# Optimization experiments

Hardware: AMD Instinct MI355X
Metric: run time of the kernel (lower is better)

## Reference

```python
import jax, jax.numpy as jnp
import numpy as np

K = 16  # number of nearest neighbors (includes self)


def setup_inputs() -> dict:
    key = jax.random.key(0)
    ks = jax.random.split(key, 12)
    B, N, D = 8, 4096, 3
    H, G, A = 128, 16, 32
    s = lambda k, shape, fan: jax.random.normal(k, shape, jnp.float32) / np.sqrt(fan)
    return {
        "pos": jax.random.normal(ks[0], (B, N, D), jnp.float32),
        "goal": jax.random.normal(ks[1], (B, G), jnp.float32),
        # local_encoder: Linear(2D,64) -> ReLU -> Linear(64,H) -> ReLU
        "W1": s(ks[2], (2 * D, 64), 2 * D), "b1": jnp.zeros((64,), jnp.float32),
        "W2": s(ks[3], (64, H), 64), "b2": jnp.zeros((H,), jnp.float32),
        # FiLM conditioning from goal
        "Wg": s(ks[4], (G, H), G), "bg": jnp.zeros((H,), jnp.float32),
        "Wb": s(ks[5], (G, H), G), "bb": jnp.zeros((H,), jnp.float32),
        # to_affordance: Linear(H, A) -> ReLU
        "Wa": s(ks[6], (H, A), H), "ba": jnp.zeros((A,), jnp.float32),
    }


def reference(pos, goal, W1, b1, W2, b2, Wg, bg, Wb, bb, Wa, ba):
    # pos: (B, N, D)
    # Squared pairwise distances via the Gram trick (monotone in true distance,
    # so k-NN indices match torch.cdist + topk(largest=False)).
    sq = jnp.sum(pos * pos, axis=-1)                      # (B, N)
    d2 = sq[:, :, None] + sq[:, None, :] - 2.0 * jnp.einsum("bnd,bmd->bnm", pos, pos)
    d2 = jnp.maximum(d2, 0.0)                             # (B, N, N)
    _, idx = jax.lax.top_k(-d2, K)                        # smallest K -> (B, N, K)

    # Gather neighbor coordinates: neighbors[b, i, j] = pos[b, idx[b, i, j]]
    neighbors = jax.vmap(lambda p, i: p[i])(pos, idx)     # (B, N, K, D)
    # mean of relative offsets == mean(neighbors) - pos
    local_context = neighbors.mean(axis=2) - pos          # (B, N, D)

    x = jnp.concatenate([pos, local_context], axis=-1)    # (B, N, 2D)
    h = jax.nn.relu(x @ W1 + b1)
    features = jax.nn.relu(h @ W2 + b2)                   # (B, N, H)

    gamma = (goal @ Wg + bg)[:, None, :]                  # (B, 1, H)
    beta = (goal @ Wb + bb)[:, None, :]
    features = gamma * features + beta

    return jax.nn.relu(features @ Wa + ba)                # (B, N, A)
```

## Files before the change

### kernel.cpp

```cpp
#include <hip/hip_runtime.h>
#include <math.h>

#define NPTS 4096
#define QTR  1024
#define KNN  16
#define H_DIM 128
#define HID1 64
#define A_DIM 32
#define G_DIM 16

#define BUF_ROWS 16
#define FLUSH_AT 8
#define GROUP 8
#define EPS 3e-4f

typedef unsigned long long u64;


#define SWAP_ST(k)                                                         \
    { bool sw_ = best[k] < best[k-1];                                      \
      u64 lo_ = sw_ ? best[k] : best[k-1];                                 \
      u64 hi_ = sw_ ? best[k-1] : best[k];                                 \
      best[k-1] = lo_; best[k] = hi_; }

#define INSERT_KEY(keyv)                                                   \
    { best[15] = (keyv);                                                   \
      SWAP_ST(15) SWAP_ST(14) SWAP_ST(13) SWAP_ST(12) SWAP_ST(11)          \
      SWAP_ST(10) SWAP_ST(9)  SWAP_ST(8)  SWAP_ST(7)  SWAP_ST(6)           \
      SWAP_ST(5)  SWAP_ST(4)  SWAP_ST(3)  SWAP_ST(2)  SWAP_ST(1) }

#define CE(i, j)                                                           \
    { u64 x_ = m[i], y_ = m[j];                                            \
      bool sw_ = y_ < x_;                                                  \
      m[i] = sw_ ? y_ : x_; m[j] = sw_ ? x_ : y_; }

__global__ __launch_bounds__(256, 2) void knn_film_mlp_kernel(
    const float* __restrict__ pos, const float* __restrict__ goal,
    const float* __restrict__ W1, const float* __restrict__ b1,
    const float* __restrict__ W2, const float* __restrict__ b2,
    const float* __restrict__ Wg, const float* __restrict__ bg,
    const float* __restrict__ Wb, const float* __restrict__ bb,
    const float* __restrict__ Wa, const float* __restrict__ ba,
    float* __restrict__ out)
{
    __shared__ float4 sp[NPTS];
    __shared__ unsigned short bufi[BUF_ROWS][256];
    __shared__ unsigned short pubi[2][KNN][64];
    __shared__ float gam[H_DIM], bet[H_DIM];
    __shared__ float4 lc[64];

    const int tid  = threadIdx.x;
    const int lane = tid & 63;
    const int wid  = tid >> 6;
    const int b     = blockIdx.x >> 6;
    const int chunk = blockIdx.x & 63;
    const int q     = chunk * 64 + lane;

    const float* pb = pos + (size_t)b * NPTS * 3;
    for (int j = tid; j < NPTS; j += 256) {
        float x = pb[j * 3 + 0];
        float y = pb[j * 3 + 1];
        float z = pb[j * 3 + 2];
        float sq = __fadd_rn(__fadd_rn(__fmul_rn(x, x), __fmul_rn(y, y)),
                             __fmul_rn(z, z));
        sp[j] = make_float4(x, y, z, sq);
    }
    if (tid < H_DIM) {
        const float* gl = goal + b * G_DIM;
        float sg = bg[tid];
        float sb = bb[tid];
        #pragma unroll
        for (int g = 0; g < G_DIM; ++g) {
            float gv = gl[g];
            sg = fmaf(gv, Wg[g * H_DIM + tid], sg);
            sb = fmaf(gv, Wb[g * H_DIM + tid], sb);
        }
        gam[tid] = sg;
        bet[tid] = sb;
    }
    __syncthreads();

    const float4 me = sp[q];
    const float nx = -2.0f * me.x, ny = -2.0f * me.y, nz = -2.0f * me.z;

#define CAND_D2(c)                                                             \
    __fsub_rn(__fadd_rn(me.w, (c).w),                                          \
              __fmul_rn(2.0f,                                                  \
                        __fadd_rn(__fadd_rn(__fmul_rn(me.x, (c).x),            \
                                            __fmul_rn(me.y, (c).y)),           \
                                  __fmul_rn(me.z, (c).z))))

    u64 best[KNN];
    #pragma unroll
    for (int k = 0; k < KNN; ++k) best[k] = 0xFFFFFFFFFFFFFFFFull;

    const int jbase = wid * QTR;

    for (int j = jbase; j < jbase + KNN; ++j) {
        float4 c = sp[j];
        float d2 = fmaxf(CAND_D2(c), 0.0f);
        u64 key = ((u64)__float_as_uint(d2) << 32) | (unsigned)j;
        INSERT_KEY(key);
    }
    float thrm = (__uint_as_float((unsigned)(best[15] >> 32)) - me.w) + EPS;
    int cnt = 0;

#define FLUSH()                                                                \
    { int t = 0;                                                               \
      while (__any(t < cnt)) {                                                 \
          int j = bufi[t][tid] & (NPTS - 1);                                   \
          float4 c = sp[j];                                                    \
          float d2 = fmaxf(CAND_D2(c), 0.0f);                                  \
          u64 key = ((u64)__float_as_uint(d2) << 32) | (unsigned)j;            \
          if ((t < cnt) && (key < best[15])) { INSERT_KEY(key); }              \
          t++;                                                                 \
      }                                                                        \
      cnt = 0;                                                                 \
      thrm = (__uint_as_float((unsigned)(best[15] >> 32)) - me.w) + EPS; }

    for (int j0 = jbase + KNN; j0 < jbase + QTR; j0 += GROUP) {
        #pragma unroll
        for (int jj = 0; jj < GROUP; ++jj) {
            const int j = j0 + jj;
            float4 c = sp[j];
            float s = fmaf(nx, c.x, fmaf(ny, c.y, fmaf(nz, c.z, c.w)));
            bool pass = s < thrm;
            bufi[cnt][tid] = (unsigned short)j;
            cnt += pass ? 1 : 0;
        }
        if (__any(cnt >= FLUSH_AT)) FLUSH();
    }
    FLUSH();

    float* pubd = (float*)&bufi[0][0];

#define PUBLISH(l)                                                             \
    _Pragma("unroll")                                                          \
    for (int k = 0; k < KNN; ++k) {                                            \
        pubd[(l) * 1024 + k * 64 + lane] =                                     \
            __uint_as_float((unsigned)(best[k] >> 32));                        \
        pubi[l][k][lane] = (unsigned short)(best[k] & 0xFFFFu);                \
    }

#define MERGE_FROM(l)                                                          \
    { u64 m[16];                                                               \
      _Pragma("unroll")                                                        \
      for (int i = 0; i < 16; ++i) {                                           \
          int kk = 15 - i;                                                     \
          u64 bk = ((u64)__float_as_uint(pubd[(l) * 1024 + kk * 64 + lane])    \
                    << 32) | (u64)pubi[l][kk][lane];                           \
          m[i] = best[i] < bk ? best[i] : bk;                                  \
      }                                                                        \
      CE(0,8) CE(1,9) CE(2,10) CE(3,11) CE(4,12) CE(5,13) CE(6,14) CE(7,15)    \
      CE(0,4) CE(1,5) CE(2,6) CE(3,7) CE(8,12) CE(9,13) CE(10,14) CE(11,15)    \
      CE(0,2) CE(1,3) CE(4,6) CE(5,7) CE(8,10) CE(9,11) CE(12,14) CE(13,15)    \
      CE(0,1) CE(2,3) CE(4,5) CE(6,7) CE(8,9) CE(10,11) CE(12,13) CE(14,15)    \
      _Pragma("unroll")                                                        \
      for (int i = 0; i < 16; ++i) best[i] = m[i]; }

    __syncthreads();
    if (wid >= 2) PUBLISH(wid - 2);
    __syncthreads();
    if (wid == 0) MERGE_FROM(0);
    if (wid == 1) { MERGE_FROM(1); PUBLISH(1); }
    __syncthreads();
    if (wid == 0) {
        MERGE_FROM(1);
        float sx = 0.0f, sy = 0.0f, sz = 0.0f;
        #pragma unroll
        for (int k = 0; k < KNN; ++k) {
            float4 nb = sp[(unsigned)(best[k] & 0xFFFFu)];
            sx += nb.x; sy += nb.y; sz += nb.z;
        }
        const float inv = 1.0f / (float)KNN;
        lc[lane] = make_float4(sx * inv - me.x, sy * inv - me.y,
                               sz * inv - me.z, 0.0f);
    }
    __syncthreads();

    {
        float4 l4 = lc[lane];
        const float x3 = l4.x, x4 = l4.y, x5 = l4.z;
        float h[HID1];
        #pragma unroll
        for (int c = 0; c < HID1; ++c) {
            float a = b1[c];
            a = fmaf(me.x, W1[0 * HID1 + c], a);
            a = fmaf(me.y, W1[1 * HID1 + c], a);
            a = fmaf(me.z, W1[2 * HID1 + c], a);
            a = fmaf(x3,   W1[3 * HID1 + c], a);
            a = fmaf(x4,   W1[4 * HID1 + c], a);
            a = fmaf(x5,   W1[5 * HID1 + c], a);
            h[c] = fmaxf(a, 0.0f);
        }
        float acc[A_DIM];
        #pragma unroll
        for (int a = 0; a < A_DIM; ++a) acc[a] = 0.0f;
        const int ci = wid;
        #pragma unroll 4
        for (int cc = 0; cc < 32; ++cc) {
            const int c = ci * 32 + cc;
            float s = b2[c];
            #pragma unroll
            for (int k = 0; k < HID1; ++k) s = fmaf(h[k], W2[k * H_DIM + c], s);
            float f = fmaf(gam[c], fmaxf(s, 0.0f), bet[c]);
            const float* wac = Wa + c * A_DIM;
            #pragma unroll
            for (int a = 0; a < A_DIM; ++a) acc[a] = fmaf(f, wac[a], acc[a]);
        }
        float* P = (float*)sp;
        #pragma unroll
        for (int a = 0; a < A_DIM; ++a) P[(ci * A_DIM + a) * 64 + lane] = acc[a];
    }
    __syncthreads();

    {
        const float* P = (const float*)sp;
        const int qi = tid >> 2, a0 = (tid & 3) * 8;
        float o[8];
        #pragma unroll
        for (int a = 0; a < 8; ++a) {
            float ssum = ba[a0 + a];
            #pragma unroll
            for (int c4 = 0; c4 < 4; ++c4)
                ssum += P[(c4 * A_DIM + a0 + a) * 64 + qi];
            o[a] = fmaxf(ssum, 0.0f);
        }
        float4* op4 = (float4*)(out + ((size_t)b * NPTS + chunk * 64 + qi) * A_DIM + a0);
        op4[0] = make_float4(o[0], o[1], o[2], o[3]);
        op4[1] = make_float4(o[4], o[5], o[6], o[7]);
    }
#undef CAND_D2
#undef FLUSH
#undef PUBLISH
#undef MERGE_FROM
}

extern "C" void kernel_launch(void* const* d_in, const int* in_sizes, int n_in,
                              void* d_out, int out_size, void* d_ws, size_t ws_size,
                              hipStream_t stream) {
    const float* pos  = (const float*)d_in[0];
    const float* goal = (const float*)d_in[1];
    const float* W1   = (const float*)d_in[2];
    const float* b1   = (const float*)d_in[3];
    const float* W2   = (const float*)d_in[4];
    const float* b2   = (const float*)d_in[5];
    const float* Wg   = (const float*)d_in[6];
    const float* bg   = (const float*)d_in[7];
    const float* Wb   = (const float*)d_in[8];
    const float* bb   = (const float*)d_in[9];
    const float* Wa   = (const float*)d_in[10];
    const float* ba   = (const float*)d_in[11];
    float* out = (float*)d_out;

    const int B = in_sizes[0] / (NPTS * 3);
    dim3 grid(B * 64);
    dim3 block(256);
    hipLaunchKernelGGL(knn_film_mlp_kernel, grid, block, 0, stream,
                       pos, goal, W1, b1, W2, b2, Wg, bg, Wb, bb, Wa, ba, out);
}
```

Baseline: 262.7 us.

## Split candidate scan across eight waves with shared atomic kNN threshold

Doubles the block to 512 threads so each of eight waves scans an eighth of the candidate points for the same 64 queries. The per-query pruning threshold now lives in shared memory and is tightened with atomicMin, so every wave prunes with the best bound found by any wave. Partial top-16 lists are merged through a double-buffered publish/merge chain, and the MLP and reduction stages are re-split across eight waves. Buffer and group sizes shrink to fit LDS. In exchange there is a longer serial merge chain, more barriers, and register pressure under launch_bounds(512,4).

```diff
diff --git a/kernel.cpp b/kernel.cpp
--- a/kernel.cpp
+++ b/kernel.cpp
@@ -2,19 +2,20 @@
 #include <math.h>
 
 #define NPTS 4096
-#define QTR  1024
+#define EIG  512
 #define KNN  16
 #define H_DIM 128
 #define HID1 64
 #define A_DIM 32
 #define G_DIM 16
 
-#define BUF_ROWS 16
-#define FLUSH_AT 8
-#define GROUP 8
+#define BUF_ROWS 7
+#define FLUSH_AT 4
+#define GROUP 4
 #define EPS 3e-4f
 
 typedef unsigned long long u64;
+typedef unsigned short u16;
 
 
 #define SWAP_ST(k)                                                         \
@@ -34,7 +35,7 @@
       bool sw_ = y_ < x_;                                                  \
       m[i] = sw_ ? y_ : x_; m[j] = sw_ ? x_ : y_; }
 
-__global__ __launch_bounds__(256, 2) void knn_film_mlp_kernel(
+__global__ __launch_bounds__(512, 4) void knn_film_mlp_kernel(
     const float* __restrict__ pos, const float* __restrict__ goal,
     const float* __restrict__ W1, const float* __restrict__ b1,
     const float* __restrict__ W2, const float* __restrict__ b2,
@@ -44,10 +45,9 @@
     float* __restrict__ out)
 {
     __shared__ float4 sp[NPTS];
-    __shared__ unsigned short bufi[BUF_ROWS][256];
-    __shared__ unsigned short pubi[2][KNN][64];
-    __shared__ float gam[H_DIM], bet[H_DIM];
-    __shared__ float4 lc[64];
+    __shared__ int    pool[12544 / 4];
+    __shared__ float  gam[H_DIM], bet[H_DIM];
+    __shared__ float  lcx[64], lcy[64], lcz[64];
 
     const int tid  = threadIdx.x;
     const int lane = tid & 63;
@@ -56,8 +56,13 @@
     const int chunk = blockIdx.x & 63;
     const int q     = chunk * 64 + lane;
 
+    u16* sbuf = (u16*)pool;
+    int* sthr = pool + (12288 / 4);
+
+    if (tid < 64) sthr[tid] = 0x7F800000;
+
     const float* pb = pos + (size_t)b * NPTS * 3;
-    for (int j = tid; j < NPTS; j += 256) {
+    for (int j = tid; j < NPTS; j += 512) {
         float x = pb[j * 3 + 0];
         float y = pb[j * 3 + 1];
         float z = pb[j * 3 + 2];
@@ -94,7 +99,7 @@
     #pragma unroll
     for (int k = 0; k < KNN; ++k) best[k] = 0xFFFFFFFFFFFFFFFFull;
 
-    const int jbase = wid * QTR;
+    const int jbase = wid * EIG;
 
     for (int j = jbase; j < jbase + KNN; ++j) {
         float4 c = sp[j];
@@ -102,13 +107,14 @@
         u64 key = ((u64)__float_as_uint(d2) << 32) | (unsigned)j;
         INSERT_KEY(key);
     }
-    float thrm = (__uint_as_float((unsigned)(best[15] >> 32)) - me.w) + EPS;
+    atomicMin(&sthr[lane], (int)(unsigned)(best[15] >> 32));
+
     int cnt = 0;
 
 #define FLUSH()                                                                \
     { int t = 0;                                                               \
       while (__any(t < cnt)) {                                                 \
-          int j = bufi[t][tid] & (NPTS - 1);                                   \
+          int j = sbuf[t * 512 + tid] & (NPTS - 1);                            \
           float4 c = sp[j];                                                    \
           float d2 = fmaxf(CAND_D2(c), 0.0f);                                  \
           u64 key = ((u64)__float_as_uint(d2) << 32) | (unsigned)j;            \
@@ -116,39 +122,42 @@
           t++;                                                                 \
       }                                                                        \
       cnt = 0;                                                                 \
-      thrm = (__uint_as_float((unsigned)(best[15] >> 32)) - me.w) + EPS; }
-
-    for (int j0 = jbase + KNN; j0 < jbase + QTR; j0 += GROUP) {
+      unsigned b15_ = (unsigned)(best[15] >> 32);                              \
+      if (b15_ < 0x7F800000u) atomicMin(&sthr[lane], (int)b15_); }
+
+    for (int j0 = jbase + KNN; j0 < jbase + EIG; j0 += GROUP) {
+        float sv = __int_as_float(sthr[lane]);
+        float tm = (sv - me.w) + EPS;
         #pragma unroll
         for (int jj = 0; jj < GROUP; ++jj) {
             const int j = j0 + jj;
             float4 c = sp[j];
             float s = fmaf(nx, c.x, fmaf(ny, c.y, fmaf(nz, c.z, c.w)));
-            bool pass = s < thrm;
-            bufi[cnt][tid] = (unsigned short)j;
+            bool pass = s < tm;
+            sbuf[cnt * 512 + tid] = (u16)j;
             cnt += pass ? 1 : 0;
         }
         if (__any(cnt >= FLUSH_AT)) FLUSH();
     }
     FLUSH();
 
-    float* pubd = (float*)&bufi[0][0];
-
-#define PUBLISH(l)                                                             \
+#define PUBLISH(s)                                                             \
     _Pragma("unroll")                                                          \
     for (int k = 0; k < KNN; ++k) {                                            \
-        pubd[(l) * 1024 + k * 64 + lane] =                                     \
+        ((float*)pool)[(s) * 1536 + k * 64 + lane] =                           \
             __uint_as_float((unsigned)(best[k] >> 32));                        \
-        pubi[l][k][lane] = (unsigned short)(best[k] & 0xFFFFu);                \
-    }
-
-#define MERGE_FROM(l)                                                          \
+        ((u16*)pool)[(s) * 3072 + 2048 + k * 64 + lane] =                      \
+            (u16)(best[k] & 0xFFFFu);                                          \
+    }
+
+#define MERGE_FROM(s)                                                          \
     { u64 m[16];                                                               \
       _Pragma("unroll")                                                        \
       for (int i = 0; i < 16; ++i) {                                           \
           int kk = 15 - i;                                                     \
-          u64 bk = ((u64)__float_as_uint(pubd[(l) * 1024 + kk * 64 + lane])    \
-                    << 32) | (u64)pubi[l][kk][lane];                           \
+          u64 bk = ((u64)__float_as_uint(                                      \
+                        ((float*)pool)[(s) * 1536 + kk * 64 + lane]) << 32)    \
+                 | (u64)((u16*)pool)[(s) * 3072 + 2048 + kk * 64 + lane];      \
           m[i] = best[i] < bk ? best[i] : bk;                                  \
       }                                                                        \
       CE(0,8) CE(1,9) CE(2,10) CE(3,11) CE(4,12) CE(5,13) CE(6,14) CE(7,15)    \
@@ -159,13 +168,28 @@
       for (int i = 0; i < 16; ++i) best[i] = m[i]; }
 
     __syncthreads();
-    if (wid >= 2) PUBLISH(wid - 2);
+    if (wid == 1) PUBLISH(0);
+    if (wid == 2) PUBLISH(1);
     __syncthreads();
     if (wid == 0) MERGE_FROM(0);
-    if (wid == 1) { MERGE_FROM(1); PUBLISH(1); }
+    __syncthreads();
+    if (wid == 0) MERGE_FROM(1);
+    if (wid == 3) PUBLISH(0);
+    __syncthreads();
+    if (wid == 0) MERGE_FROM(0);
+    if (wid == 4) PUBLISH(1);
+    __syncthreads();
+    if (wid == 0) MERGE_FROM(1);
+    if (wid == 5) PUBLISH(0);
+    __syncthreads();
+    if (wid == 0) MERGE_FROM(0);
+    if (wid == 6) PUBLISH(1);
+    __syncthreads();
+    if (wid == 0) MERGE_FROM(1);
+    if (wid == 7) PUBLISH(0);
     __syncthreads();
     if (wid == 0) {
-        MERGE_FROM(1);
+        MERGE_FROM(0);
         float sx = 0.0f, sy = 0.0f, sz = 0.0f;
         #pragma unroll
         for (int k = 0; k < KNN; ++k) {
@@ -173,14 +197,14 @@
             sx += nb.x; sy += nb.y; sz += nb.z;
         }
         const float inv = 1.0f / (float)KNN;
-        lc[lane] = make_float4(sx * inv - me.x, sy * inv - me.y,
-                               sz * inv - me.z, 0.0f);
+        lcx[lane] = sx * inv - me.x;
+        lcy[lane] = sy * inv - me.y;
+        lcz[lane] = sz * inv - me.z;
     }
     __syncthreads();
 
     {
-        float4 l4 = lc[lane];
-        const float x3 = l4.x, x4 = l4.y, x5 = l4.z;
+        const float x3 = lcx[lane], x4 = lcy[lane], x5 = lcz[lane];
         float h[HID1];
         #pragma unroll
         for (int c = 0; c < HID1; ++c) {
@@ -196,10 +220,10 @@
         float acc[A_DIM];
         #pragma unroll
         for (int a = 0; a < A_DIM; ++a) acc[a] = 0.0f;
-        const int ci = wid;
+        const int c0 = wid * 16;
         #pragma unroll 4
-        for (int cc = 0; cc < 32; ++cc) {
-            const int c = ci * 32 + cc;
+        for (int cc = 0; cc < 16; ++cc) {
+            const int c = c0 + cc;
             float s = b2[c];
             #pragma unroll
             for (int k = 0; k < HID1; ++k) s = fmaf(h[k], W2[k * H_DIM + c], s);
@@ -210,25 +234,25 @@
         }
         float* P = (float*)sp;
         #pragma unroll
-        for (int a = 0; a < A_DIM; ++a) P[(ci * A_DIM + a) * 64 + lane] = acc[a];
+        for (int a = 0; a < A_DIM; ++a) P[(wid * A_DIM + a) * 64 + lane] = acc[a];
     }
     __syncthreads();
 
     {
         const float* P = (const float*)sp;
-        const int qi = tid >> 2, a0 = (tid & 3) * 8;
-        float o[8];
-        #pragma unroll
-        for (int a = 0; a < 8; ++a) {
-            float ssum = ba[a0 + a];
+        const int qi = tid & 63;
+        const int a0 = (tid >> 6) * 4;
+        float o[4];
+        #pragma unroll
+        for (int i = 0; i < 4; ++i) {
+            float ssum = ba[a0 + i];
             #pragma unroll
-            for (int c4 = 0; c4 < 4; ++c4)
-                ssum += P[(c4 * A_DIM + a0 + a) * 64 + qi];
-            o[a] = fmaxf(ssum, 0.0f);
+            for (int w = 0; w < 8; ++w)
+                ssum += P[(w * A_DIM + a0 + i) * 64 + qi];
+            o[i] = fmaxf(ssum, 0.0f);
         }
         float4* op4 = (float4*)(out + ((size_t)b * NPTS + chunk * 64 + qi) * A_DIM + a0);
-        op4[0] = make_float4(o[0], o[1], o[2], o[3]);
-        op4[1] = make_float4(o[4], o[5], o[6], o[7]);
+        *op4 = make_float4(o[0], o[1], o[2], o[3]);
     }
 #undef CAND_D2
 #undef FLUSH
@@ -255,7 +279,7 @@
 
     const int B = in_sizes[0] / (NPTS * 3);
     dim3 grid(B * 64);
-    dim3 block(256);
+    dim3 block(512);
     hipLaunchKernelGGL(knn_film_mlp_kernel, grid, block, 0, stream,
                        pos, goal, W1, b1, W2, b2, Wg, bg, Wb, bb, Wa, ba, out);
 }
```

Result: slower. 282.7 us (+7.6%).

## Share pruning threshold across waves via LDS atomicMin and use bitmask windows

Applied to the files above, without the earlier changes.

Swaps the per-thread candidate buffer and flush loop for 16-candidate windows that collect passing candidates into a bitmask and insert them right away. The four waves scanning different quarters of the point set for the same query now share a running k-th-distance threshold through an LDS atomicMin, so each wave prunes against the tightest bound found so far. The aim is fewer insertion-sort calls and less shared-memory buffer traffic. In exchange it adds an atomic and an LDS threshold read per window, and wave divergence inside the mask loop.

```diff
diff --git a/kernel.cpp b/kernel.cpp
--- a/kernel.cpp
+++ b/kernel.cpp
@@ -9,12 +9,13 @@
 #define A_DIM 32
 #define G_DIM 16
 
-#define BUF_ROWS 16
-#define FLUSH_AT 8
-#define GROUP 8
+#define WARMUP 16
+#define WSZ 16
+#define NWIN ((QTR - WARMUP) / WSZ)
 #define EPS 3e-4f
 
 typedef unsigned long long u64;
+typedef unsigned short u16;
 
 
 #define SWAP_ST(k)                                                         \
@@ -44,10 +45,11 @@
     float* __restrict__ out)
 {
     __shared__ float4 sp[NPTS];
-    __shared__ unsigned short bufi[BUF_ROWS][256];
-    __shared__ unsigned short pubi[2][KNN][64];
-    __shared__ float gam[H_DIM], bet[H_DIM];
-    __shared__ float4 lc[64];
+    __shared__ float  pubd[2][KNN][64];
+    __shared__ u16    pubi[2][KNN][64];
+    __shared__ float  gam[H_DIM], bet[H_DIM];
+    __shared__ float  lcx[64], lcy[64], lcz[64];
+    __shared__ int    sthr[64];
 
     const int tid  = threadIdx.x;
     const int lane = tid & 63;
@@ -55,6 +57,8 @@
     const int b     = blockIdx.x >> 6;
     const int chunk = blockIdx.x & 63;
     const int q     = chunk * 64 + lane;
+
+    if (tid < 64) sthr[tid] = 0x7F800000;
 
     const float* pb = pos + (size_t)b * NPTS * 3;
     for (int j = tid; j < NPTS; j += 256) {
@@ -96,59 +100,54 @@
 
     const int jbase = wid * QTR;
 
-    for (int j = jbase; j < jbase + KNN; ++j) {
+    for (int j = jbase; j < jbase + WARMUP; ++j) {
         float4 c = sp[j];
         float d2 = fmaxf(CAND_D2(c), 0.0f);
         u64 key = ((u64)__float_as_uint(d2) << 32) | (unsigned)j;
         INSERT_KEY(key);
     }
-    float thrm = (__uint_as_float((unsigned)(best[15] >> 32)) - me.w) + EPS;
-    int cnt = 0;
-
-#define FLUSH()                                                                \
-    { int t = 0;                                                               \
-      while (__any(t < cnt)) {                                                 \
-          int j = bufi[t][tid] & (NPTS - 1);                                   \
-          float4 c = sp[j];                                                    \
-          float d2 = fmaxf(CAND_D2(c), 0.0f);                                  \
-          u64 key = ((u64)__float_as_uint(d2) << 32) | (unsigned)j;            \
-          if ((t < cnt) && (key < best[15])) { INSERT_KEY(key); }              \
-          t++;                                                                 \
-      }                                                                        \
-      cnt = 0;                                                                 \
-      thrm = (__uint_as_float((unsigned)(best[15] >> 32)) - me.w) + EPS; }
-
-    for (int j0 = jbase + KNN; j0 < jbase + QTR; j0 += GROUP) {
-        #pragma unroll
-        for (int jj = 0; jj < GROUP; ++jj) {
-            const int j = j0 + jj;
-            float4 c = sp[j];
+    atomicMin(&sthr[lane], (int)(unsigned)(best[15] >> 32));
+
+    for (int w = 0; w < NWIN; ++w) {
+        const int wbase = jbase + WARMUP + w * WSZ;
+        const float tm = (__int_as_float(sthr[lane]) - me.w) + EPS;
+        unsigned mask = 0u;
+        #pragma unroll
+        for (int u = 0; u < WSZ; ++u) {
+            float4 c = sp[wbase + u];
             float s = fmaf(nx, c.x, fmaf(ny, c.y, fmaf(nz, c.z, c.w)));
-            bool pass = s < thrm;
-            bufi[cnt][tid] = (unsigned short)j;
-            cnt += pass ? 1 : 0;
-        }
-        if (__any(cnt >= FLUSH_AT)) FLUSH();
-    }
-    FLUSH();
-
-    float* pubd = (float*)&bufi[0][0];
-
-#define PUBLISH(l)                                                             \
+            if (s < tm) mask |= (1u << u);
+        }
+        if (__any(mask != 0u)) {
+            while (__any(mask != 0u)) {
+                bool act = (mask != 0u);
+                int bit = __ffs(mask) - 1;
+                mask &= mask - 1;
+                int j = (wbase + bit) & (NPTS - 1);
+                float4 c = sp[j];
+                float d2 = fmaxf(CAND_D2(c), 0.0f);
+                u64 key = ((u64)__float_as_uint(d2) << 32) | (unsigned)j;
+                if (act && key < best[15]) { INSERT_KEY(key); }
+            }
+            unsigned b15 = (unsigned)(best[15] >> 32);
+            if (b15 < 0x7F800000u) atomicMin(&sthr[lane], (int)b15);
+        }
+    }
+
+#define PUBLISH(s)                                                             \
     _Pragma("unroll")                                                          \
     for (int k = 0; k < KNN; ++k) {                                            \
-        pubd[(l) * 1024 + k * 64 + lane] =                                     \
-            __uint_as_float((unsigned)(best[k] >> 32));                        \
-        pubi[l][k][lane] = (unsigned short)(best[k] & 0xFFFFu);                \
-    }
-
-#define MERGE_FROM(l)                                                          \
+        pubd[s][k][lane] = __uint_as_float((unsigned)(best[k] >> 32));         \
+        pubi[s][k][lane] = (u16)(best[k] & 0xFFFFu);                           \
+    }
+
+#define MERGE_FROM(s)                                                          \
     { u64 m[16];                                                               \
       _Pragma("unroll")                                                        \
       for (int i = 0; i < 16; ++i) {                                           \
           int kk = 15 - i;                                                     \
-          u64 bk = ((u64)__float_as_uint(pubd[(l) * 1024 + kk * 64 + lane])    \
-                    << 32) | (u64)pubi[l][kk][lane];                           \
+          u64 bk = ((u64)__float_as_uint(pubd[s][kk][lane]) << 32)             \
+                 | (u64)pubi[s][kk][lane];                                     \
           m[i] = best[i] < bk ? best[i] : bk;                                  \
       }                                                                        \
       CE(0,8) CE(1,9) CE(2,10) CE(3,11) CE(4,12) CE(5,13) CE(6,14) CE(7,15)    \
@@ -173,14 +172,14 @@
             sx += nb.x; sy += nb.y; sz += nb.z;
         }
         const float inv = 1.0f / (float)KNN;
-        lc[lane] = make_float4(sx * inv - me.x, sy * inv - me.y,
-                               sz * inv - me.z, 0.0f);
+        lcx[lane] = sx * inv - me.x;
+        lcy[lane] = sy * inv - me.y;
+        lcz[lane] = sz * inv - me.z;
     }
     __syncthreads();
 
     {
-        float4 l4 = lc[lane];
-        const float x3 = l4.x, x4 = l4.y, x5 = l4.z;
+        const float x3 = lcx[lane], x4 = lcy[lane], x5 = lcz[lane];
         float h[HID1];
         #pragma unroll
         for (int c = 0; c < HID1; ++c) {
@@ -196,10 +195,10 @@
         float acc[A_DIM];
         #pragma unroll
         for (int a = 0; a < A_DIM; ++a) acc[a] = 0.0f;
-        const int ci = wid;
+        const int c0 = wid * 32;
         #pragma unroll 4
         for (int cc = 0; cc < 32; ++cc) {
-            const int c = ci * 32 + cc;
+            const int c = c0 + cc;
             float s = b2[c];
             #pragma unroll
             for (int k = 0; k < HID1; ++k) s = fmaf(h[k], W2[k * H_DIM + c], s);
@@ -210,7 +209,7 @@
         }
         float* P = (float*)sp;
         #pragma unroll
-        for (int a = 0; a < A_DIM; ++a) P[(ci * A_DIM + a) * 64 + lane] = acc[a];
+        for (int a = 0; a < A_DIM; ++a) P[(wid * A_DIM + a) * 64 + lane] = acc[a];
     }
     __syncthreads();
 
@@ -231,7 +230,6 @@
         op4[1] = make_float4(o[4], o[5], o[6], o[7]);
     }
 #undef CAND_D2
-#undef FLUSH
 #undef PUBLISH
 #undef MERGE_FROM
 }
```

Result: slower. 271.1 us (+3.2%).
